# Kernel tuning notes

Hardware: AMD Instinct MI355X
Metric: run time of the kernel (lower is better)

The kernel has to match this reference:

```python
import jax, jax.numpy as jnp
import numpy as np

INF = 10000.0


def setup_inputs() -> dict:
    key = jax.random.key(0)
    ks = jax.random.split(key, 4)
    bs, seqlen, hidden = 8, 512, 768
    head_size, heads = 64, 12
    inputs = jax.random.normal(ks[0], (bs, seqlen, hidden), dtype=jnp.float32)
    attention_mask = jnp.ones((bs, seqlen), dtype=jnp.int32)
    W1 = jax.random.normal(ks[1], (hidden, head_size * 2), dtype=jnp.float32) * 0.02
    b1 = jnp.zeros((head_size * 2,), dtype=jnp.float32)
    W2 = jax.random.normal(ks[2], (head_size * 2, heads * 2), dtype=jnp.float32) * 0.02
    b2 = jnp.zeros((heads * 2,), dtype=jnp.float32)
    return {"inputs": inputs, "attention_mask": attention_mask,
            "W1": W1, "b1": b1, "W2": W2, "b2": b2}


def _rope(t, sin, cos):
    # t: [b, s, d]; sin/cos: [s, d//2]
    t1, t2 = t[..., 0::2], t[..., 1::2]
    return jnp.stack([t1 * cos - t2 * sin, t1 * sin + t2 * cos], axis=-1).reshape(t.shape)


def reference(inputs, attention_mask, W1, b1, W2, b2):
    bs, seqlen = inputs.shape[:2]
    head_size = W1.shape[1] // 2
    x = inputs @ W1 + b1                      # [b, s, 2*head_size]
    qw, kw = x[..., 0::2], x[..., 1::2]       # [b, s, head_size] each
    # rotary embedding (computed like the buffer in the torch module)
    pos = jnp.arange(seqlen, dtype=jnp.float32)
    inv_freq = 1.0 / (10000.0 ** (jnp.arange(0, head_size, 2, dtype=jnp.float32) / head_size))
    freqs = pos[:, None] * inv_freq[None, :]  # [s, head_size//2]
    sin, cos = jnp.sin(freqs), jnp.cos(freqs)
    qw = _rope(qw, sin, cos)
    kw = _rope(kw, sin, cos)
    logits = jnp.einsum('bmd,bnd->bmn', qw, kw) / (head_size ** 0.5)  # [b, s, s]
    bias = (x @ W2 + b2).transpose(0, 2, 1) / 2.0                      # [b, 2*heads, s]
    logits = logits[:, None] + bias[:, ::2, None, :] + bias[:, 1::2, :, None]  # [b, h, s, s]
    am = attention_mask.astype(logits.dtype)
    mask = 1.0 - am[:, None, None, :] * am[:, None, :, None]           # [b, 1, s, s]
    logits = logits - mask * INF
    # tril mask: positions with end < start (j < i)
    idx = jnp.arange(seqlen)
    tril = (idx[None, :] < idx[:, None]).astype(logits.dtype)[None, None]  # [1, 1, s, s]
    logits = logits - tril * INF
    mask_out = jnp.logical_or(mask.astype(bool),
                              jnp.broadcast_to(tril.astype(bool), (bs, 1, seqlen, seqlen)))
    return logits, mask_out
```

## Files before the change

### kernel.cpp

```cpp
#include <hip/hip_runtime.h>

#define BSZ 8
#define SEQ 512
#define HID 768
#define N1 128
#define N2 24
#define HS 64
#define HEADS 12
#define INFV 10000.0f

typedef __attribute__((ext_vector_type(8))) short s8b;
typedef __attribute__((ext_vector_type(4))) float f32x4;

__device__ __forceinline__ unsigned short f2bf(float f) {
    union { float f; unsigned int u; } c; c.f = f;
    unsigned int u = c.u;
    u += 0x7FFFu + ((u >> 16) & 1u);
    return (unsigned short)(u >> 16);
}

__global__ __launch_bounds__(128) void k0_prep(
    const float* __restrict__ W1, const float* __restrict__ W2,
    unsigned short* __restrict__ W1T, float* __restrict__ W2T,
    float2* __restrict__ sct)
{
    const int tid = threadIdx.x;
    const int bid = blockIdx.x;
    if (bid < 96) {
        const int c = tid;
        const int k0 = bid * 8;
        unsigned short v[8];
#pragma unroll
        for (int i = 0; i < 8; ++i)
            v[i] = f2bf(W1[(size_t)(k0 + i) * N1 + c]);
        unsigned short* dst = W1T + (size_t)c * HID + k0;
#pragma unroll
        for (int i = 0; i < 8; ++i) dst[i] = v[i];
    } else if (bid == 96) {
#pragma unroll
        for (int c = 0; c < N2; ++c)
            W2T[c * N1 + tid] = W2[tid * N2 + c];
    } else {
        const float C = 0.4152410118609203f;
        int e0 = (bid - 97) * 512 + tid * 4;
#pragma unroll
        for (int u = 0; u < 4; ++u) {
            int e = e0 + u;
            int m = e >> 5, j = e & 31;
            float ang = (float)m * exp2f(-(float)j * C);
            float sv, cv;
            sincosf(ang, &sv, &cv);
            sct[e] = make_float2(sv, cv);
        }
    }
}

__global__ __launch_bounds__(512, 4) void k1_proj(
    const float* __restrict__ inp, const unsigned short* __restrict__ W1T,
    const float* __restrict__ b1, const float* __restrict__ W2T,
    const float* __restrict__ b2, const float2* __restrict__ sct,
    float* __restrict__ qw, float* __restrict__ kwT,
    float* __restrict__ bP0, float* __restrict__ bP1)
{
    __shared__ unsigned short aF[96 * 16 * 8];
    __shared__ float ps[16][64];
    __shared__ float xs[16][72];
    __shared__ float kT[32][17];

    const int tid = threadIdx.x;
    const int rt = blockIdx.x >> 1;
    const int ch = blockIdx.x & 1;
    const int row0 = rt * 16;
    const int b = row0 >> 9;
    const int m0 = row0 & 511;

    {
        const float4* src = (const float4*)(inp + (size_t)row0 * HID);
#pragma unroll
        for (int i = 0; i < 6; ++i) {
            int f4 = tid + i * 512;
            int r = f4 / 192;
            int c4 = f4 % 192;
            float4 v = src[f4];
            int chunk = c4 >> 1;
            int half = c4 & 1;
            ushort4 w;
            w.x = f2bf(v.x); w.y = f2bf(v.y); w.z = f2bf(v.z); w.w = f2bf(v.w);
            *(ushort4*)&aF[(chunk * 16 + r) * 8 + half * 4] = w;
        }
    }
    __syncthreads();

    const int wv = tid >> 6;
    const int ln = tid & 63;
    const int lr = ln & 15;
    const int lg = ln >> 4;
    const int w3 = wv & 3;
    const int kh = wv >> 2;
    const int cg = ch * 64 + w3 * 16 + lr;

    const s8b* bp = (const s8b*)W1T + ((size_t)cg * 96 + kh * 48 + lg);

    f32x4 acc = {0.f, 0.f, 0.f, 0.f};
#pragma unroll
    for (int kc = 0; kc < 12; ++kc) {
        s8b a = *(const s8b*)&aF[(((kh * 12 + kc) * 4 + lg) * 16 + lr) * 8];
        acc = __builtin_amdgcn_mfma_f32_16x16x32_bf16(a, bp[kc * 4], acc, 0, 0, 0);
    }

    if (kh == 1) {
#pragma unroll
        for (int g = 0; g < 4; ++g) ps[lg * 4 + g][w3 * 16 + lr] = acc[g];
    }
    __syncthreads();
    if (kh == 0) {
        float b1v = b1[cg];
#pragma unroll
        for (int g = 0; g < 4; ++g)
            xs[lg * 4 + g][w3 * 16 + lr] = acc[g] + ps[lg * 4 + g][w3 * 16 + lr] + b1v;
    }
    __syncthreads();

    if (tid < 16 * N2) {
        int r = tid / N2, c = tid - r * N2;
        const float* xr = &xs[r][0];
        const float* wr = W2T + c * N1 + ch * 64;
        float dot = (ch == 0) ? b2[c] : 0.0f;
#pragma unroll
        for (int k4 = 0; k4 < 16; ++k4) {
            float4 xv = *(const float4*)&xr[k4 * 4];
            float4 wv2 = *(const float4*)&wr[k4 * 4];
            dot = fmaf(xv.x, wv2.x, dot); dot = fmaf(xv.y, wv2.y, dot);
            dot = fmaf(xv.z, wv2.z, dot); dot = fmaf(xv.w, wv2.w, dot);
        }
        float* bP = ch ? bP1 : bP0;
        bP[(size_t)(b * N2 + c) * SEQ + m0 + r] = dot * 0.5f;
    }

    if (tid < 256) {
        const int r = tid >> 4, jj = tid & 15;
        const int j = ch * 16 + jj;
        const int m = m0 + r;
        float2 sc = sct[m * 32 + j];
        float4 xv = *(const float4*)&xs[r][4 * jj];
        float rq0 = xv.x * sc.y - xv.z * sc.x;
        float rq1 = xv.x * sc.x + xv.z * sc.y;
        float rk0 = xv.y * sc.y - xv.w * sc.x;
        float rk1 = xv.y * sc.x + xv.w * sc.y;
        *(float2*)(qw + (size_t)(b * SEQ + m) * HS + 2 * j) = make_float2(rq0, rq1);
        kT[2 * jj][r]     = rk0;
        kT[2 * jj + 1][r] = rk1;
    }
    __syncthreads();

    if (tid < 256) {
        int dl = tid >> 3, q = tid & 7;
        float2 v = *(const float2*)&kT[dl][2 * q];
        *(float2*)(kwT + (size_t)(b * HS + ch * 32 + dl) * SEQ + m0 + 2 * q) = v;
    }
}

__global__ __launch_bounds__(256) void k2_out(
    const float* __restrict__ qw, const float* __restrict__ kwT,
    const float* __restrict__ bP0, const float* __restrict__ bP1,
    const int* __restrict__ am, float* __restrict__ out)
{
    __shared__ float q_lds[8][HS];
    __shared__ float bo[8][HEADS];
    __shared__ int amm[8];

    const int tid = threadIdx.x;
    const int b = blockIdx.x >> 6;
    const int m0 = (blockIdx.x & 63) * 8;

#pragma unroll
    for (int i = 0; i < 2; ++i) {
        int idx = tid + i * 256;
        q_lds[idx >> 6][idx & 63] = qw[(size_t)(b * SEQ + m0) * HS + idx];
    }
    if (tid < 96) {
        int r = tid / 12, h = tid - r * 12;
        size_t ix = (size_t)(b * N2 + 2 * h + 1) * SEQ + m0 + r;
        bo[r][h] = bP0[ix] + bP1[ix];
    }
    if (tid < 8) amm[tid] = am[b * SEQ + m0 + tid];
    __syncthreads();

    const int n0 = tid * 2;
    float qk0[8] = {0, 0, 0, 0, 0, 0, 0, 0};
    float qk1[8] = {0, 0, 0, 0, 0, 0, 0, 0};

#pragma unroll
    for (int dc = 0; dc < 2; ++dc) {
        float2 kn[32];
#pragma unroll
        for (int d = 0; d < 32; ++d)
            kn[d] = *(const float2*)&kwT[(size_t)(b * HS + dc * 32 + d) * SEQ + n0];
#pragma unroll
        for (int r = 0; r < 8; ++r) {
#pragma unroll
            for (int d4 = 0; d4 < 8; ++d4) {
                float4 qv = *(const float4*)&q_lds[r][dc * 32 + d4 * 4];
                qk0[r] = fmaf(qv.x, kn[d4 * 4 + 0].x, qk0[r]);
                qk0[r] = fmaf(qv.y, kn[d4 * 4 + 1].x, qk0[r]);
                qk0[r] = fmaf(qv.z, kn[d4 * 4 + 2].x, qk0[r]);
                qk0[r] = fmaf(qv.w, kn[d4 * 4 + 3].x, qk0[r]);
                qk1[r] = fmaf(qv.x, kn[d4 * 4 + 0].y, qk1[r]);
                qk1[r] = fmaf(qv.y, kn[d4 * 4 + 1].y, qk1[r]);
                qk1[r] = fmaf(qv.z, kn[d4 * 4 + 2].y, qk1[r]);
                qk1[r] = fmaf(qv.w, kn[d4 * 4 + 3].y, qk1[r]);
            }
        }
    }

    const int amn0 = am[b * SEQ + n0];
    const int amn1 = am[b * SEQ + n0 + 1];
    float pen0[8], pen1[8];
    float2 mo[8];
#pragma unroll
    for (int r = 0; r < 8; ++r) {
        int m = m0 + r;
        float msk0 = (1.0f - (float)(amn0 * amm[r])) * INFV;
        float msk1 = (1.0f - (float)(amn1 * amm[r])) * INFV;
        pen0[r] = msk0 + ((n0 < m) ? INFV : 0.0f);
        pen1[r] = msk1 + ((n0 + 1 < m) ? INFV : 0.0f);
        bool b0 = (amn0 * amm[r] != 1) || (n0 < m);
        bool b1m = (amn1 * amm[r] != 1) || (n0 + 1 < m);
        mo[r].x = b0 ? 1.0f : 0.0f;
        mo[r].y = b1m ? 1.0f : 0.0f;
    }

    float2 be[HEADS];
#pragma unroll
    for (int h = 0; h < HEADS; ++h) {
        size_t ix = (size_t)(b * N2 + 2 * h) * SEQ + n0;
        float2 e0 = *(const float2*)&bP0[ix];
        float2 e1 = *(const float2*)&bP1[ix];
        be[h] = make_float2(e0.x + e1.x, e0.y + e1.y);
    }

    const size_t obase = (size_t)b * HEADS * SEQ * SEQ + n0;
#pragma unroll
    for (int h = 0; h < HEADS; ++h) {
#pragma unroll
        for (int r = 0; r < 8; ++r) {
            float2 v;
            v.x = fmaf(qk0[r], 0.125f, be[h].x + bo[r][h]) - pen0[r];
            v.y = fmaf(qk1[r], 0.125f, be[h].y + bo[r][h]) - pen1[r];
            *(float2*)&out[obase + ((size_t)h * SEQ + m0 + r) * SEQ] = v;
        }
    }
    const size_t mbase = (size_t)BSZ * HEADS * SEQ * SEQ
                       + ((size_t)b * SEQ + m0) * SEQ + n0;
#pragma unroll
    for (int r = 0; r < 8; ++r)
        *(float2*)&out[mbase + (size_t)r * SEQ] = mo[r];
}

extern "C" void kernel_launch(void* const* d_in, const int* in_sizes, int n_in,
                              void* d_out, int out_size, void* d_ws, size_t ws_size,
                              hipStream_t stream) {
    const float* inp = (const float*)d_in[0];
    const int*   am  = (const int*)d_in[1];
    const float* W1  = (const float*)d_in[2];
    const float* b1  = (const float*)d_in[3];
    const float* W2  = (const float*)d_in[4];
    const float* b2  = (const float*)d_in[5];

    float* ws    = (float*)d_ws;
    float* qw    = ws;
    float* kwT   = ws + 262144;
    float* bP0   = ws + 524288;
    float* bP1   = ws + 622592;
    unsigned short* W1T = (unsigned short*)(ws + 720896);
    float* W2T   = ws + 819200;
    float2* sct  = (float2*)(ws + 822272);

    float* out = (float*)d_out;

    hipLaunchKernelGGL(k0_prep, dim3(129), dim3(128), 0, stream,
                       W1, W2, W1T, W2T, sct);
    hipLaunchKernelGGL(k1_proj, dim3(512), dim3(512), 0, stream,
                       inp, W1T, b1, W2T, b2, sct, qw, kwT, bP0, bP1);
    hipLaunchKernelGGL(k2_out, dim3(4096 / 8), dim3(256), 0, stream,
                       qw, kwT, bP0, bP1, am, out);
}
```

Measured before the change: 49.84 us.

## Fuse weight prep and rope table into projection kernel, swizzle LDS A tile

```diff
diff --git a/kernel.cpp b/kernel.cpp
--- a/kernel.cpp
+++ b/kernel.cpp
@@ -19,46 +19,19 @@
     return (unsigned short)(u >> 16);
 }
 
-__global__ __launch_bounds__(128) void k0_prep(
-    const float* __restrict__ W1, const float* __restrict__ W2,
-    unsigned short* __restrict__ W1T, float* __restrict__ W2T,
-    float2* __restrict__ sct)
-{
-    const int tid = threadIdx.x;
-    const int bid = blockIdx.x;
-    if (bid < 96) {
-        const int c = tid;
-        const int k0 = bid * 8;
-        unsigned short v[8];
-#pragma unroll
-        for (int i = 0; i < 8; ++i)
-            v[i] = f2bf(W1[(size_t)(k0 + i) * N1 + c]);
-        unsigned short* dst = W1T + (size_t)c * HID + k0;
-#pragma unroll
-        for (int i = 0; i < 8; ++i) dst[i] = v[i];
-    } else if (bid == 96) {
-#pragma unroll
-        for (int c = 0; c < N2; ++c)
-            W2T[c * N1 + tid] = W2[tid * N2 + c];
-    } else {
-        const float C = 0.4152410118609203f;
-        int e0 = (bid - 97) * 512 + tid * 4;
-#pragma unroll
-        for (int u = 0; u < 4; ++u) {
-            int e = e0 + u;
-            int m = e >> 5, j = e & 31;
-            float ang = (float)m * exp2f(-(float)j * C);
-            float sv, cv;
-            sincosf(ang, &sv, &cv);
-            sct[e] = make_float2(sv, cv);
-        }
-    }
-}
+__device__ __forceinline__ s8b loadB(const float* __restrict__ wsrc) {
+    union { s8b v; unsigned short u[8]; } r;
+#pragma unroll
+    for (int i = 0; i < 8; ++i) r.u[i] = f2bf(wsrc[i * N1]);
+    return r.v;
+}
+
+#define ASLOT(chunk, r) (((chunk) * 16 + ((r) ^ ((chunk) & 7))) * 8)
 
 __global__ __launch_bounds__(512, 4) void k1_proj(
-    const float* __restrict__ inp, const unsigned short* __restrict__ W1T,
-    const float* __restrict__ b1, const float* __restrict__ W2T,
-    const float* __restrict__ b2, const float2* __restrict__ sct,
+    const float* __restrict__ inp, const float* __restrict__ W1,
+    const float* __restrict__ b1, const float* __restrict__ W2,
+    const float* __restrict__ b2,
     float* __restrict__ qw, float* __restrict__ kwT,
     float* __restrict__ bP0, float* __restrict__ bP1)
 {
@@ -86,7 +59,7 @@
             int half = c4 & 1;
             ushort4 w;
             w.x = f2bf(v.x); w.y = f2bf(v.y); w.z = f2bf(v.z); w.w = f2bf(v.w);
-            *(ushort4*)&aF[(chunk * 16 + r) * 8 + half * 4] = w;
+            *(ushort4*)&aF[ASLOT(chunk, r) + half * 4] = w;
         }
     }
     __syncthreads();
@@ -99,14 +72,21 @@
     const int kh = wv >> 2;
     const int cg = ch * 64 + w3 * 16 + lr;
 
-    const s8b* bp = (const s8b*)W1T + ((size_t)cg * 96 + kh * 48 + lg);
+    const float* wbase = W1 + (size_t)(kh * 384 + lg * 8) * N1 + cg;
 
     f32x4 acc = {0.f, 0.f, 0.f, 0.f};
-#pragma unroll
-    for (int kc = 0; kc < 12; ++kc) {
-        s8b a = *(const s8b*)&aF[(((kh * 12 + kc) * 4 + lg) * 16 + lr) * 8];
-        acc = __builtin_amdgcn_mfma_f32_16x16x32_bf16(a, bp[kc * 4], acc, 0, 0, 0);
-    }
+    s8b bA = loadB(wbase);
+    s8b bB = loadB(wbase + 32 * N1);
+
+#define AFRAG(kc) (*(const s8b*)&aF[ASLOT((kh * 12 + (kc)) * 4 + lg, lr)])
+#pragma unroll
+    for (int kc = 0; kc < 12; kc += 2) {
+        acc = __builtin_amdgcn_mfma_f32_16x16x32_bf16(AFRAG(kc), bA, acc, 0, 0, 0);
+        if (kc + 2 < 12) bA = loadB(wbase + (size_t)(kc + 2) * 32 * N1);
+        acc = __builtin_amdgcn_mfma_f32_16x16x32_bf16(AFRAG(kc + 1), bB, acc, 0, 0, 0);
+        if (kc + 3 < 12) bB = loadB(wbase + (size_t)(kc + 3) * 32 * N1);
+    }
+#undef AFRAG
 
     if (kh == 1) {
 #pragma unroll
@@ -123,16 +103,11 @@
 
     if (tid < 16 * N2) {
         int r = tid / N2, c = tid - r * N2;
-        const float* xr = &xs[r][0];
-        const float* wr = W2T + c * N1 + ch * 64;
+        const float* w2p = W2 + (size_t)(ch * 64) * N2 + c;
         float dot = (ch == 0) ? b2[c] : 0.0f;
-#pragma unroll
-        for (int k4 = 0; k4 < 16; ++k4) {
-            float4 xv = *(const float4*)&xr[k4 * 4];
-            float4 wv2 = *(const float4*)&wr[k4 * 4];
-            dot = fmaf(xv.x, wv2.x, dot); dot = fmaf(xv.y, wv2.y, dot);
-            dot = fmaf(xv.z, wv2.z, dot); dot = fmaf(xv.w, wv2.w, dot);
-        }
+#pragma unroll 8
+        for (int kl = 0; kl < 64; ++kl)
+            dot = fmaf(xs[r][kl], w2p[kl * N2], dot);
         float* bP = ch ? bP1 : bP0;
         bP[(size_t)(b * N2 + c) * SEQ + m0 + r] = dot * 0.5f;
     }
@@ -141,12 +116,15 @@
         const int r = tid >> 4, jj = tid & 15;
         const int j = ch * 16 + jj;
         const int m = m0 + r;
-        float2 sc = sct[m * 32 + j];
+        const float C = 0.4152410118609203f;
+        float invf = exp2f(-(float)j * C);
+        float ang = (float)m * invf;
+        float sv = __sinf(ang), cv = __cosf(ang);
         float4 xv = *(const float4*)&xs[r][4 * jj];
-        float rq0 = xv.x * sc.y - xv.z * sc.x;
-        float rq1 = xv.x * sc.x + xv.z * sc.y;
-        float rk0 = xv.y * sc.y - xv.w * sc.x;
-        float rk1 = xv.y * sc.x + xv.w * sc.y;
+        float rq0 = xv.x * cv - xv.z * sv;
+        float rq1 = xv.x * sv + xv.z * cv;
+        float rk0 = xv.y * cv - xv.w * sv;
+        float rk1 = xv.y * sv + xv.w * cv;
         *(float2*)(qw + (size_t)(b * SEQ + m) * HS + 2 * j) = make_float2(rq0, rq1);
         kT[2 * jj][r]     = rk0;
         kT[2 * jj + 1][r] = rk1;
@@ -272,16 +250,11 @@
     float* kwT   = ws + 262144;
     float* bP0   = ws + 524288;
     float* bP1   = ws + 622592;
-    unsigned short* W1T = (unsigned short*)(ws + 720896);
-    float* W2T   = ws + 819200;
-    float2* sct  = (float2*)(ws + 822272);
 
     float* out = (float*)d_out;
 
-    hipLaunchKernelGGL(k0_prep, dim3(129), dim3(128), 0, stream,
-                       W1, W2, W1T, W2T, sct);
     hipLaunchKernelGGL(k1_proj, dim3(512), dim3(512), 0, stream,
-                       inp, W1T, b1, W2T, b2, sct, qw, kwT, bP0, bP1);
+                       inp, W1, b1, W2, b2, qw, kwT, bP0, bP1);
     hipLaunchKernelGGL(k2_out, dim3(4096 / 8), dim3(256), 0, stream,
                        qw, kwT, bP0, bP1, am, out);
 }
```

New measurement: 40.10 us. 19.5% less time.
